# Optimization experiments

Hardware: AMD Instinct MI355X
Metric: run time of the kernel (lower is better)

## Reference

```python
import jax, jax.numpy as jnp
import numpy as np

N, NF, D, GH, E, B = 4096, 128, 64, 64, 32768, 32
NG, STEPS = 3, 3  # n_gcn, set2set processing steps


def setup_inputs() -> dict:
    key = jax.random.key(0)
    ks = iter(jax.random.split(key, 64))
    nrm = lambda shape: jax.random.normal(next(ks), shape, dtype=jnp.float32) * 0.05
    inp = {
        'x': jax.random.normal(next(ks), (N, NF), dtype=jnp.float32),
        'edge_attr': jax.random.uniform(next(ks), (E,), dtype=jnp.float32),
        'edge_idx': jax.random.randint(next(ks), (2, E), 0, N),
        'batch_map': jnp.sort(jax.random.randint(next(ks), (N,), 0, B)),
        # pre-GC MLP: NF->D, D->D, D->D (ReLU each)
        'pre_W0': nrm((NF, D)), 'pre_b0': nrm((D,)),
        'pre_W1': nrm((D, D)), 'pre_b1': nrm((D,)),
        'pre_W2': nrm((D, D)), 'pre_b2': nrm((D,)),
        # NNConv edge nets (stacked over NG layers): 1->GH->D*D
        'enn_W1': nrm((NG, 1, GH)), 'enn_b1': nrm((NG, GH)),
        'enn_W2': nrm((NG, GH, D * D)), 'enn_b2': nrm((NG, D * D)),
        'root_W': nrm((NG, D, D)), 'conv_b': nrm((NG, D)),
        # GRU(D, D) per layer, gate order r,z,n (torch), stored transposed for x@W
        'gru_Wih': nrm((NG, D, 3 * D)), 'gru_Whh': nrm((NG, D, 3 * D)),
        'gru_bih': nrm((NG, 3 * D)), 'gru_bhh': nrm((NG, 3 * D)),
        # Set2Set LSTM: input 2D -> hidden D, gate order i,f,g,o (torch)
        's2s_Wih': nrm((2 * D, 4 * D)), 's2s_Whh': nrm((D, 4 * D)),
        's2s_bih': nrm((4 * D,)), 's2s_bhh': nrm((4 * D,)),
        # post-GC MLP: 2D->D, D->D, D->D (ReLU each), then D->1
        'post_W0': nrm((2 * D, D)), 'post_b0': nrm((D,)),
        'post_W1': nrm((D, D)), 'post_b1': nrm((D,)),
        'post_W2': nrm((D, D)), 'post_b2': nrm((D,)),
        'post_W3': nrm((D, 1)), 'post_b3': nrm((1,)),
    }
    return inp


def _forward(x, edge_attr, pre_W0, pre_b0, pre_W1, pre_b1, pre_W2, pre_b2,
             enn_W1, enn_b1, enn_W2, enn_b2, root_W, conv_b,
             gru_Wih, gru_Whh, gru_bih, gru_bhh,
             s2s_Wih, s2s_Whh, s2s_bih, s2s_bhh,
             post_W0, post_b0, post_W1, post_b1, post_W2, post_b2,
             post_W3, post_b3, edge_idx, batch_map):
    relu, sig = jax.nn.relu, jax.nn.sigmoid
    # pre-GC layers
    out = relu(x @ pre_W0 + pre_b0)
    out = relu(out @ pre_W1 + pre_b1)
    out = relu(out @ pre_W2 + pre_b2)  # [N, D]

    src, dst = edge_idx[0], edge_idx[1]
    deg = jax.ops.segment_sum(jnp.ones((E,), out.dtype), dst, num_segments=N)
    deg = jnp.maximum(deg, 1.0)
    ea = edge_attr[:, None]  # view(-1, 1)

    for l in range(NG):
        h = out
        # NNConv: per-edge weight matrix from edge MLP
        We = relu(ea @ enn_W1[l] + enn_b1[l])              # [E, GH]
        We = (We @ enn_W2[l] + enn_b2[l]).reshape(E, D, D)  # [E, D, D]
        msg = jnp.einsum('ei,eio->eo', out[src], We)        # [E, D]
        agg = jax.ops.segment_sum(msg, dst, num_segments=N) / deg[:, None]
        conv = relu(agg + out @ root_W[l] + conv_b[l])
        # single-step GRU update (torch gate order r, z, n)
        gi = conv @ gru_Wih[l] + gru_bih[l]
        gh = h @ gru_Whh[l] + gru_bhh[l]
        i_r, i_z, i_n = jnp.split(gi, 3, axis=-1)
        h_r, h_z, h_n = jnp.split(gh, 3, axis=-1)
        r = sig(i_r + h_r)
        z = sig(i_z + h_z)
        n = jnp.tanh(i_n + r * h_n)
        out = (1.0 - z) * n + z * h

    # Set2Set pooling (early)
    q_star = jnp.zeros((B, 2 * D), out.dtype)
    hh = jnp.zeros((B, D), out.dtype)
    cc = jnp.zeros((B, D), out.dtype)
    for _ in range(STEPS):
        gates = q_star @ s2s_Wih + s2s_bih + hh @ s2s_Whh + s2s_bhh
        gi_, gf, gg, go = jnp.split(gates, 4, axis=-1)
        cc = sig(gf) * cc + sig(gi_) * jnp.tanh(gg)
        hh = sig(go) * jnp.tanh(cc)
        q = hh
        e = jnp.sum(out * q[batch_map], axis=-1)                    # [N]
        m = jax.ops.segment_max(e, batch_map, num_segments=B)
        a = jnp.exp(e - m[batch_map])
        den = jax.ops.segment_sum(a, batch_map, num_segments=B)
        a = a / den[batch_map]
        r_read = jax.ops.segment_sum(a[:, None] * out, batch_map, num_segments=B)
        q_star = jnp.concatenate([q, r_read], axis=-1)              # [B, 2D]

    # post-GC layers
    y = relu(q_star @ post_W0 + post_b0)
    y = relu(y @ post_W1 + post_b1)
    y = relu(y @ post_W2 + post_b2)
    y = y @ post_W3 + post_b3  # [B, 1]
    return y


def reference(x, edge_attr, edge_idx, batch_map, pre_W0, pre_b0, pre_W1, pre_b1,
              pre_W2, pre_b2, enn_W1, enn_b1, enn_W2, enn_b2, root_W, conv_b,
              gru_Wih, gru_Whh, gru_bih, gru_bhh, s2s_Wih, s2s_Whh, s2s_bih,
              s2s_bhh, post_W0, post_b0, post_W1, post_b1, post_W2, post_b2,
              post_W3, post_b3):
    return _forward(x, edge_attr, pre_W0, pre_b0, pre_W1, pre_b1, pre_W2, pre_b2,
                    enn_W1, enn_b1, enn_W2, enn_b2, root_W, conv_b,
                    gru_Wih, gru_Whh, gru_bih, gru_bhh,
                    s2s_Wih, s2s_Whh, s2s_bih, s2s_bhh,
                    post_W0, post_b0, post_W1, post_b1, post_W2, post_b2,
                    post_W3, post_b3, edge_idx, batch_map)
```

## Files before the change

kernel.cpp:

```cpp
#include <hip/hip_runtime.h>
#include <hip/hip_bf16.h>
#include <string.h>

#define NN   4096
#define NE   32768
#define NB   32
#define BKT  64

typedef __attribute__((ext_vector_type(8))) short short8;
typedef __attribute__((ext_vector_type(4))) float f4;

__device__ __forceinline__ float sigf(float x) { return 1.0f / (1.0f + __expf(-x)); }
__device__ __forceinline__ float bf2f(short s) {
    union { unsigned u; float f; } x;
    x.u = ((unsigned)(unsigned short)s) << 16;
    return x.f;
}
__device__ __forceinline__ short f2bf(float f) {
    __hip_bfloat16 h = __float2bfloat16(f);
    short s;
    memcpy(&s, &h, sizeof(short));
    return s;
}

__global__ __launch_bounds__(256) void k_setup(const float* __restrict__ x,
        const float* __restrict__ W0, const float* __restrict__ b0,
        const float* __restrict__ W1, const float* __restrict__ b1,
        const float* __restrict__ W2, const float* __restrict__ b2,
        const float* __restrict__ enn_W2, __hip_bfloat16* __restrict__ W2T,
        float* __restrict__ out, int* cnt_src, int* cnt_dst, int* bstart, int* bend) {
    int bid = blockIdx.x, t = threadIdx.x;
    if (bid < 32) {
        int i = bid * 256 + t;
        if (i < NN) cnt_src[i] = 0;
        else cnt_dst[i - NN] = 0;
        if (i < NB) { bstart[i] = 0x7FFFFFFF; bend[i] = 0; }
    } else if (bid < 224) {
        __shared__ __hip_bfloat16 tile[64 * 65];
        size_t base = (size_t)(bid - 32) * 4096;
        for (int i = t; i < 4096; i += 256) {
            int k = i >> 6, o = i & 63;
            tile[o * 65 + k] = __float2bfloat16(enn_W2[base + i]);
        }
        __syncthreads();
        for (int i = t; i < 4096; i += 256) {
            int o = i >> 6, k = i & 63;
            W2T[base + i] = tile[o * 65 + k];
        }
    } else {
        __shared__ float xr[4][128], ha[4][64], hb[4][64];
        int w = t >> 6, j = t & 63;
        int n = (bid - 224) * 4 + w;
        xr[w][j] = x[(size_t)n * 128 + j];
        xr[w][64 + j] = x[(size_t)n * 128 + 64 + j];
        float s = b0[j];
        #pragma unroll 8
        for (int k = 0; k < 128; ++k) s = fmaf(xr[w][k], W0[k * 64 + j], s);
        ha[w][j] = fmaxf(s, 0.f);
        s = b1[j];
        #pragma unroll 8
        for (int k = 0; k < 64; ++k) s = fmaf(ha[w][k], W1[k * 64 + j], s);
        hb[w][j] = fmaxf(s, 0.f);
        s = b2[j];
        #pragma unroll 8
        for (int k = 0; k < 64; ++k) s = fmaf(hb[w][k], W2[k * 64 + j], s);
        out[(size_t)n * 64 + j] = fmaxf(s, 0.f);
    }
}

__global__ __launch_bounds__(256, 4) void k_gemmPbt(const float* __restrict__ out,
        const __hip_bfloat16* __restrict__ W2T_l, const float* __restrict__ b2l,
        __hip_bfloat16* __restrict__ P, float* __restrict__ BT, float* __restrict__ agg,
        const int* __restrict__ eidx, const float* __restrict__ ea,
        const int* __restrict__ bm, int* cnt_src, int* cnt_dst,
        int* csr_dst, float* csr_ea, int* bstart, int* bend) {
    int bid = blockIdx.x, t = threadIdx.x;
    if (bid < 1024) {
        int mtile32 = bid >> 3, gchunk = bid & 7;
        int wave = t >> 6, lane = t & 63;
        int laneM = lane & 15, quad = lane >> 4;
        int rowhalf = wave & 1, subpair = wave >> 1;
        int arow = mtile32 * 32 + rowhalf * 16 + laneM;
        const float* Arow = out + (size_t)arow * 64;
        f4 af0 = *(const f4*)(Arow + quad * 8);
        f4 af1 = *(const f4*)(Arow + quad * 8 + 4);
        f4 af2 = *(const f4*)(Arow + 32 + quad * 8);
        f4 af3 = *(const f4*)(Arow + 32 + quad * 8 + 4);
        short8 a0, a1;
        #pragma unroll
        for (int j = 0; j < 4; ++j) {
            a0[j] = f2bf(af0[j]); a0[4 + j] = f2bf(af1[j]);
            a1[j] = f2bf(af2[j]); a1[4 + j] = f2bf(af3[j]);
        }
        #pragma unroll
        for (int sp = 0; sp < 2; ++sp) {
            int o0 = (subpair * 2 + sp) * 16;
            float accs[4][8];
            #pragma unroll
            for (int gg = 0; gg < 8; ++gg) {
                const __hip_bfloat16* Bt = W2T_l + (size_t)(gchunk * 8 + gg) * 4096;
                short8 b0v = *(const short8*)(Bt + (o0 + laneM) * 64 + quad * 8);
                short8 b1v = *(const short8*)(Bt + (o0 + laneM) * 64 + 32 + quad * 8);
                f4 acc = {0.f, 0.f, 0.f, 0.f};
                acc = __builtin_amdgcn_mfma_f32_16x16x32_bf16(a0, b0v, acc, 0, 0, 0);
                acc = __builtin_amdgcn_mfma_f32_16x16x32_bf16(a1, b1v, acc, 0, 0, 0);
                #pragma unroll
                for (int r = 0; r < 4; ++r) accs[r][gg] = acc[r];
            }
            int rowg = mtile32 * 32 + rowhalf * 16 + quad * 4;
            #pragma unroll
            for (int r = 0; r < 4; ++r) {
                short8 sv;
                #pragma unroll
                for (int j = 0; j < 8; ++j)
                    sv[j] = f2bf(accs[r][j]);
                *(short8*)(P + (size_t)(rowg + r) * 4096 + gchunk * 512
                             + (o0 + laneM) * 8) = sv;
            }
        }
    } else if (bid < 2048) {
        __shared__ float sh[4][64];
        int w = t >> 6, j = t & 63;
        int n = (bid - 1024) * 4 + w;
        sh[w][j] = out[(size_t)n * 64 + j];
        agg[(size_t)n * 64 + j] = 0.f;
        __syncthreads();
        float s = 0.f;
        #pragma unroll 8
        for (int k = 0; k < 64; ++k) s = fmaf(sh[w][k], b2l[k * 64 + j], s);
        BT[(size_t)n * 64 + j] = s;
    } else {
        int e = (bid - 2048) * 256 + t;
        if (e < NE) {
            int s = eidx[e];
            int d = eidx[NE + e];
            int slot = atomicAdd(&cnt_src[s], 1);
            if (slot < BKT) {
                csr_dst[s * BKT + slot] = d;
                csr_ea[s * BKT + slot] = ea[e];
            }
            atomicAdd(&cnt_dst[d], 1);
        }
        if (e < NN) {
            int b = bm[e];
            atomicMin(&bstart[b], e);
            atomicMax(&bend[b], e + 1);
        }
    }
}

#define MSG_CHUNK 32
__global__ __launch_bounds__(256, 2) void k_msg(const __hip_bfloat16* __restrict__ P,
        const float* __restrict__ BT, const int* __restrict__ cnt_src,
        const int* __restrict__ csr_dst, const float* __restrict__ csr_ea,
        const float* __restrict__ W1l, const float* __restrict__ b1l,
        float* __restrict__ agg) {
    __shared__ float wlds[4][MSG_CHUNK][64];
    int t = threadIdx.x, wave = t >> 6, lane = t & 63;
    int n = blockIdx.x * 4 + wave;
    int deg = cnt_src[n];
    if (deg > BKT) deg = BKT;
    float w1v = W1l[lane], b1v = b1l[lane];
    float preg[64];
    const __hip_bfloat16* Pn = P + (size_t)n * 4096 + lane * 8;
    #pragma unroll
    for (int c = 0; c < 8; ++c) {
        short8 v = *(const short8*)(Pn + c * 512);
        #pragma unroll
        for (int j = 0; j < 8; ++j) preg[c * 8 + j] = bf2f(v[j]);
    }
    float bt = BT[(size_t)n * 64 + lane];
    const int* bdst = csr_dst + n * BKT;
    const float* bea = csr_ea + n * BKT;
    for (int c0 = 0; c0 < deg; c0 += MSG_CHUNK) {
        int cc = deg - c0; if (cc > MSG_CHUNK) cc = MSG_CHUNK;
        for (int si = 0; si < cc; ++si) {
            float eav = bea[c0 + si];
            wlds[wave][si][lane] = fmaxf(fmaf(eav, w1v, b1v), 0.f);
        }
        for (int i = 0; i < cc; ++i) {
            int dst = bdst[c0 + i];
            const float* wr = wlds[wave][i];
            float acc0 = bt, acc1 = 0.f, acc2 = 0.f, acc3 = 0.f;
            #pragma unroll
            for (int g = 0; g < 64; g += 16) {
                float4 w0 = *(const float4*)(wr + g);
                float4 w1 = *(const float4*)(wr + g + 4);
                float4 w2 = *(const float4*)(wr + g + 8);
                float4 w3 = *(const float4*)(wr + g + 12);
                acc0 = fmaf(w0.x, preg[g], acc0);
                acc0 = fmaf(w0.y, preg[g + 1], acc0);
                acc0 = fmaf(w0.z, preg[g + 2], acc0);
                acc0 = fmaf(w0.w, preg[g + 3], acc0);
                acc1 = fmaf(w1.x, preg[g + 4], acc1);
                acc1 = fmaf(w1.y, preg[g + 5], acc1);
                acc1 = fmaf(w1.z, preg[g + 6], acc1);
                acc1 = fmaf(w1.w, preg[g + 7], acc1);
                acc2 = fmaf(w2.x, preg[g + 8], acc2);
                acc2 = fmaf(w2.y, preg[g + 9], acc2);
                acc2 = fmaf(w2.z, preg[g + 10], acc2);
                acc2 = fmaf(w2.w, preg[g + 11], acc2);
                acc3 = fmaf(w3.x, preg[g + 12], acc3);
                acc3 = fmaf(w3.y, preg[g + 13], acc3);
                acc3 = fmaf(w3.z, preg[g + 14], acc3);
                acc3 = fmaf(w3.w, preg[g + 15], acc3);
            }
            float acc = (acc0 + acc1) + (acc2 + acc3);
            atomicAdd(&agg[(size_t)dst * 64 + lane], acc);
        }
    }
}

__global__ __launch_bounds__(256) void k_gru(const float* __restrict__ out,
        const float* __restrict__ agg, const int* __restrict__ cnt_dst,
        const float* __restrict__ rootW, const float* __restrict__ convb,
        const float* __restrict__ Wih, const float* __restrict__ Whh,
        const float* __restrict__ bih, const float* __restrict__ bhh,
        float* __restrict__ outn) {
    __shared__ float sh[4][64], sc[4][64];
    int t = threadIdx.x, w = t >> 6, j = t & 63;
    int n = blockIdx.x * 4 + w;
    float hj = out[(size_t)n * 64 + j];
    sh[w][j] = hj;
    int dg = cnt_dst[n];
    float invd = 1.0f / (float)(dg > 0 ? dg : 1);
    __syncthreads();
    float s = agg[(size_t)n * 64 + j] * invd + convb[j];
    #pragma unroll 8
    for (int k = 0; k < 64; ++k) s = fmaf(sh[w][k], rootW[k * 64 + j], s);
    float conv = fmaxf(s, 0.f);
    sc[w][j] = conv;
    __syncthreads();
    float gir = bih[j], giz = bih[64 + j], gin = bih[128 + j];
    float ghr = bhh[j], ghz = bhh[64 + j], ghn = bhh[128 + j];
    #pragma unroll 4
    for (int k = 0; k < 64; ++k) {
        float c = sc[w][k], h = sh[w][k];
        gir = fmaf(c, Wih[k * 192 + j], gir);
        giz = fmaf(c, Wih[k * 192 + 64 + j], giz);
        gin = fmaf(c, Wih[k * 192 + 128 + j], gin);
        ghr = fmaf(h, Whh[k * 192 + j], ghr);
        ghz = fmaf(h, Whh[k * 192 + 64 + j], ghz);
        ghn = fmaf(h, Whh[k * 192 + 128 + j], ghn);
    }
    float r = sigf(gir + ghr);
    float z = sigf(giz + ghz);
    float nn = tanhf(gin + r * ghn);
    outn[(size_t)n * 64 + j] = (1.f - z) * nn + z * hj;
}

__global__ __launch_bounds__(1024) void k_s2s_post(const float* __restrict__ out,
        const int* __restrict__ bstart, const int* __restrict__ bend,
        const float* __restrict__ Wih, const float* __restrict__ Whh,
        const float* __restrict__ bih, const float* __restrict__ bhh,
        const float* __restrict__ pW0, const float* __restrict__ pb0,
        const float* __restrict__ pW1, const float* __restrict__ pb1,
        const float* __restrict__ pW2, const float* __restrict__ pb2,
        const float* __restrict__ pW3, const float* __restrict__ pb3,
        float* __restrict__ y) {
    __shared__ float cache[192 * 65];
    __shared__ float qs[128], hh[64], cc[64], gates[256];
    __shared__ float ebuf[1024];
    __shared__ float redbuf[1024];
    __shared__ float redw[16];
    __shared__ float smax, sinv;
    __shared__ float tmp64[64];
    int t = threadIdx.x, wave = t >> 6, lane = t & 63;
    int b = blockIdx.x;
    int s0 = bstart[b], e0 = bend[b];
    int cnt = e0 - s0;
    if (cnt < 0) cnt = 0;
    if (cnt > 1024) cnt = 1024;
    int ccnt = cnt < 192 ? cnt : 192;
    for (int li = t; li < ccnt * 64; li += 1024) {
        int rowi = li >> 6, d = li & 63;
        cache[rowi * 65 + d] = out[(size_t)(s0 + rowi) * 64 + d];
    }
    int g = t & 255, seg = t >> 8;
    const float* wp;
    int kcnt;
    if (seg == 0)      { wp = Wih + g;             kcnt = 64; }
    else if (seg == 1) { wp = Wih + 64 * 256 + g;  kcnt = 64; }
    else if (seg == 2) { wp = Whh + g;             kcnt = 32; }
    else               { wp = Whh + 32 * 256 + g;  kcnt = 32; }
    float wreg[64];
    #pragma unroll
    for (int j = 0; j < 64; ++j)
        wreg[j] = (j < kcnt) ? wp[(size_t)j * 256] : 0.f;
    if (t < 128) qs[t] = 0.f;
    if (t < 64) { hh[t] = 0.f; cc[t] = 0.f; }
    __syncthreads();
    for (int step = 0; step < 3; ++step) {
        const float* vsrc = (seg == 0) ? qs : (seg == 1) ? qs + 64
                          : (seg == 2) ? hh : hh + 32;
        float partial = 0.f;
        #pragma unroll
        for (int j = 0; j < 64; ++j)
            if (j < kcnt) partial = fmaf(vsrc[j], wreg[j], partial);
        redbuf[seg * 256 + g] = partial;
        __syncthreads();
        if (t < 256)
            gates[t] = bih[t] + bhh[t] + redbuf[t] + redbuf[256 + t]
                     + redbuf[512 + t] + redbuf[768 + t];
        __syncthreads();
        if (t < 64) {
            float cn = sigf(gates[64 + t]) * cc[t] + sigf(gates[t]) * tanhf(gates[128 + t]);
            cc[t] = cn;
            hh[t] = sigf(gates[192 + t]) * tanhf(cn);
        }
        __syncthreads();
        for (int idx = t; idx < cnt; idx += 1024) {
            float s = 0.f;
            if (idx < 192) {
                const float* row = cache + idx * 65;
                #pragma unroll 8
                for (int d = 0; d < 64; ++d) s = fmaf(row[d], hh[d], s);
            } else {
                const float* row = out + (size_t)(s0 + idx) * 64;
                for (int d = 0; d < 64; ++d) s = fmaf(row[d], hh[d], s);
            }
            ebuf[idx] = s;
        }
        __syncthreads();
        float lm = (t < cnt) ? ebuf[t] : -3.0e38f;
        #pragma unroll
        for (int off = 32; off > 0; off >>= 1) lm = fmaxf(lm, __shfl_down(lm, off, 64));
        if (lane == 0) redw[wave] = lm;
        __syncthreads();
        if (t == 0) {
            float m = redw[0];
            #pragma unroll
            for (int w2 = 1; w2 < 16; ++w2) m = fmaxf(m, redw[w2]);
            smax = m;
        }
        __syncthreads();
        float m = smax;
        float av = 0.f;
        if (t < cnt) {
            av = __expf(ebuf[t] - m);
            ebuf[t] = av;
        }
        float ls = av;
        #pragma unroll
        for (int off = 32; off > 0; off >>= 1) ls += __shfl_down(ls, off, 64);
        if (lane == 0) redw[wave] = ls;
        __syncthreads();
        if (t == 0) {
            float s = 0.f;
            #pragma unroll
            for (int w2 = 0; w2 < 16; ++w2) s += redw[w2];
            sinv = (cnt > 0) ? 1.f / s : 0.f;
        }
        __syncthreads();
        float inv = sinv;
        float r = 0.f;
        for (int idx = wave; idx < cnt; idx += 16) {
            float a = ebuf[idx];
            float v = (idx < 192) ? cache[idx * 65 + lane]
                                  : out[(size_t)(s0 + idx) * 64 + lane];
            r = fmaf(a, v, r);
        }
        redbuf[wave * 64 + lane] = r;
        __syncthreads();
        if (t < 64) {
            float s = 0.f;
            #pragma unroll
            for (int w2 = 0; w2 < 16; ++w2) s += redbuf[w2 * 64 + t];
            qs[64 + t] = s * inv;
            qs[t] = hh[t];
        }
        __syncthreads();
    }
    if (t < 64) {
        float s = pb0[t];
        #pragma unroll 4
        for (int k = 0; k < 128; ++k) s = fmaf(qs[k], pW0[k * 64 + t], s);
        tmp64[t] = fmaxf(s, 0.f);
    }
    __syncthreads();
    float h1v = 0.f;
    if (t < 64) {
        float s = pb1[t];
        #pragma unroll 4
        for (int k = 0; k < 64; ++k) s = fmaf(tmp64[k], pW1[k * 64 + t], s);
        h1v = fmaxf(s, 0.f);
    }
    __syncthreads();
    if (t < 64) tmp64[t] = h1v;
    __syncthreads();
    if (t < 64) {
        float s = pb2[t];
        #pragma unroll 4
        for (int k = 0; k < 64; ++k) s = fmaf(tmp64[k], pW2[k * 64 + t], s);
        gates[t] = fmaxf(s, 0.f) * pW3[t];
    }
    __syncthreads();
    if (t == 0) {
        float yy = pb3[0];
        for (int k = 0; k < 64; ++k) yy += gates[k];
        y[b] = yy;
    }
}


extern "C" void kernel_launch(void* const* d_in, const int* in_sizes, int n_in,
                              void* d_out, int out_size, void* d_ws, size_t ws_size,
                              hipStream_t stream) {
    const float* x         = (const float*)d_in[0];
    const float* edge_attr = (const float*)d_in[1];
    const int*   edge_idx  = (const int*)d_in[2];
    const int*   batch_map = (const int*)d_in[3];
    const float* pre_W0 = (const float*)d_in[4];
    const float* pre_b0 = (const float*)d_in[5];
    const float* pre_W1 = (const float*)d_in[6];
    const float* pre_b1 = (const float*)d_in[7];
    const float* pre_W2 = (const float*)d_in[8];
    const float* pre_b2 = (const float*)d_in[9];
    const float* enn_W1 = (const float*)d_in[10];
    const float* enn_b1 = (const float*)d_in[11];
    const float* enn_W2 = (const float*)d_in[12];
    const float* enn_b2 = (const float*)d_in[13];
    const float* root_W = (const float*)d_in[14];
    const float* conv_b = (const float*)d_in[15];
    const float* gru_Wih = (const float*)d_in[16];
    const float* gru_Whh = (const float*)d_in[17];
    const float* gru_bih = (const float*)d_in[18];
    const float* gru_bhh = (const float*)d_in[19];
    const float* s2s_Wih = (const float*)d_in[20];
    const float* s2s_Whh = (const float*)d_in[21];
    const float* s2s_bih = (const float*)d_in[22];
    const float* s2s_bhh = (const float*)d_in[23];
    const float* post_W0 = (const float*)d_in[24];
    const float* post_b0 = (const float*)d_in[25];
    const float* post_W1 = (const float*)d_in[26];
    const float* post_b1 = (const float*)d_in[27];
    const float* post_W2 = (const float*)d_in[28];
    const float* post_b2 = (const float*)d_in[29];
    const float* post_W3 = (const float*)d_in[30];
    const float* post_b3 = (const float*)d_in[31];
    float* yout = (float*)d_out;

    char* wp = (char*)d_ws;
    auto take = [&](size_t bytes) -> char* {
        char* r = wp;
        wp += (bytes + 255) & ~(size_t)255;
        return r;
    };
    float* outA = (float*)take((size_t)NN * 64 * 4);
    float* outB = (float*)take((size_t)NN * 64 * 4);
    __hip_bfloat16* P = (__hip_bfloat16*)take((size_t)NN * 4096 * 2);
    float* BT  = (float*)take((size_t)NN * 64 * 4);
    float* agg = (float*)take((size_t)NN * 64 * 4);
    __hip_bfloat16* W2T = (__hip_bfloat16*)take((size_t)3 * 64 * 4096 * 2);
    int* cnt_src  = (int*)take((size_t)NN * 4);
    int* cnt_dst  = (int*)take((size_t)NN * 4);
    int* csr_dst  = (int*)take((size_t)NN * BKT * 4);
    float* csr_ea = (float*)take((size_t)NN * BKT * 4);
    int* bstart   = (int*)take((size_t)NB * 4);
    int* bend     = (int*)take((size_t)NB * 4);

    k_setup<<<1248, 256, 0, stream>>>(x, pre_W0, pre_b0, pre_W1, pre_b1, pre_W2, pre_b2,
                                      enn_W2, W2T, outA, cnt_src, cnt_dst, bstart, bend);

    float* cur = outA;
    float* nxt = outB;
    for (int l = 0; l < 3; ++l) {
        int grid = (l == 0) ? 2176 : 2048;
        k_gemmPbt<<<grid, 256, 0, stream>>>(cur, W2T + (size_t)l * 64 * 4096,
                                            enn_b2 + (size_t)l * 4096, P, BT, agg,
                                            edge_idx, edge_attr, batch_map,
                                            cnt_src, cnt_dst, csr_dst, csr_ea,
                                            bstart, bend);
        k_msg<<<NN / 4, 256, 0, stream>>>(P, BT, cnt_src, csr_dst, csr_ea,
                                          enn_W1 + l * 64, enn_b1 + l * 64, agg);
        k_gru<<<NN / 4, 256, 0, stream>>>(cur, agg, cnt_dst, root_W + l * 4096,
                                          conv_b + l * 64, gru_Wih + l * 64 * 192,
                                          gru_Whh + l * 64 * 192, gru_bih + l * 192,
                                          gru_bhh + l * 192, nxt);
        float* tmp = cur; cur = nxt; nxt = tmp;
    }
    k_s2s_post<<<NB, 1024, 0, stream>>>(cur, bstart, bend, s2s_Wih, s2s_Whh, s2s_bih,
                                        s2s_bhh, post_W0, post_b0, post_W1, post_b1,
                                        post_W2, post_b2, post_W3, post_b3, yout);
}
```

Baseline: 373.5 us.

## Fuse edge-weight GEMM into message passing, keep per-node P in LDS

```diff
diff --git a/kernel.cpp b/kernel.cpp
--- a/kernel.cpp
+++ b/kernel.cpp
@@ -6,29 +6,30 @@
 #define NE   32768
 #define NB   32
 #define BKT  64
+#define FN   8
 
 typedef __attribute__((ext_vector_type(8))) short short8;
 typedef __attribute__((ext_vector_type(4))) float f4;
 
 __device__ __forceinline__ float sigf(float x) { return 1.0f / (1.0f + __expf(-x)); }
-__device__ __forceinline__ float bf2f(short s) {
-    union { unsigned u; float f; } x;
-    x.u = ((unsigned)(unsigned short)s) << 16;
-    return x.f;
-}
 __device__ __forceinline__ short f2bf(float f) {
     __hip_bfloat16 h = __float2bfloat16(f);
     short s;
     memcpy(&s, &h, sizeof(short));
     return s;
 }
+__device__ __forceinline__ unsigned packbf2(float lo, float hi) {
+    return (unsigned)(unsigned short)f2bf(lo) | ((unsigned)(unsigned short)f2bf(hi) << 16);
+}
 
 __global__ __launch_bounds__(256) void k_setup(const float* __restrict__ x,
         const float* __restrict__ W0, const float* __restrict__ b0,
         const float* __restrict__ W1, const float* __restrict__ b1,
         const float* __restrict__ W2, const float* __restrict__ b2,
-        const float* __restrict__ enn_W2, __hip_bfloat16* __restrict__ W2T,
-        float* __restrict__ out, int* cnt_src, int* cnt_dst, int* bstart, int* bend) {
+        const float* __restrict__ enn_W2, const float* __restrict__ b2e0,
+        __hip_bfloat16* __restrict__ W2T, float* __restrict__ out,
+        float* __restrict__ BT, float* __restrict__ agg,
+        int* cnt_src, int* cnt_dst, int* bstart, int* bend) {
     int bid = blockIdx.x, t = threadIdx.x;
     if (bid < 32) {
         int i = bid * 256 + t;
@@ -64,148 +65,114 @@
         s = b2[j];
         #pragma unroll 8
         for (int k = 0; k < 64; ++k) s = fmaf(hb[w][k], W2[k * 64 + j], s);
-        out[(size_t)n * 64 + j] = fmaxf(s, 0.f);
-    }
-}
-
-__global__ __launch_bounds__(256, 4) void k_gemmPbt(const float* __restrict__ out,
-        const __hip_bfloat16* __restrict__ W2T_l, const float* __restrict__ b2l,
-        __hip_bfloat16* __restrict__ P, float* __restrict__ BT, float* __restrict__ agg,
-        const int* __restrict__ eidx, const float* __restrict__ ea,
-        const int* __restrict__ bm, int* cnt_src, int* cnt_dst,
-        int* csr_dst, float* csr_ea, int* bstart, int* bend) {
-    int bid = blockIdx.x, t = threadIdx.x;
-    if (bid < 1024) {
-        int mtile32 = bid >> 3, gchunk = bid & 7;
-        int wave = t >> 6, lane = t & 63;
-        int laneM = lane & 15, quad = lane >> 4;
-        int rowhalf = wave & 1, subpair = wave >> 1;
-        int arow = mtile32 * 32 + rowhalf * 16 + laneM;
-        const float* Arow = out + (size_t)arow * 64;
-        f4 af0 = *(const f4*)(Arow + quad * 8);
-        f4 af1 = *(const f4*)(Arow + quad * 8 + 4);
-        f4 af2 = *(const f4*)(Arow + 32 + quad * 8);
-        f4 af3 = *(const f4*)(Arow + 32 + quad * 8 + 4);
-        short8 a0, a1;
+        float val = fmaxf(s, 0.f);
+        out[(size_t)n * 64 + j] = val;
+        ha[w][j] = val;
+        agg[(size_t)n * 64 + j] = 0.f;
+        float s2 = 0.f;
+        #pragma unroll 8
+        for (int k = 0; k < 64; ++k) s2 = fmaf(ha[w][k], b2e0[k * 64 + j], s2);
+        BT[(size_t)n * 64 + j] = s2;
+    }
+}
+
+__global__ __launch_bounds__(256) void k_edges(const int* __restrict__ eidx,
+        const float* __restrict__ ea, const int* __restrict__ bm,
+        int* cnt_src, int* cnt_dst, int* csr_dst, float* csr_ea,
+        int* bstart, int* bend) {
+    int e = blockIdx.x * 256 + threadIdx.x;
+    if (e < NE) {
+        int s = eidx[e];
+        int d = eidx[NE + e];
+        int slot = atomicAdd(&cnt_src[s], 1);
+        if (slot < BKT) {
+            csr_dst[s * BKT + slot] = d;
+            csr_ea[s * BKT + slot] = ea[e];
+        }
+        atomicAdd(&cnt_dst[d], 1);
+    }
+    if (e < NN) {
+        int b = bm[e];
+        atomicMin(&bstart[b], e);
+        atomicMax(&bend[b], e + 1);
+    }
+}
+
+__global__ __launch_bounds__(256, 2) void k_fused(const float* __restrict__ out,
+        const __hip_bfloat16* __restrict__ W2T_l, const float* __restrict__ BT,
+        const int* __restrict__ cnt_src, const int* __restrict__ csr_dst,
+        const float* __restrict__ csr_ea, const float* __restrict__ W1l,
+        const float* __restrict__ b1l, float* __restrict__ agg) {
+    __shared__ unsigned Plds[FN * 32 * 64];
+    int t = threadIdx.x, wave = t >> 6, lane = t & 63;
+    int laneM = lane & 15, quad = lane >> 4;
+    int n0 = blockIdx.x * FN;
+    const float* Arow = out + (size_t)(n0 + laneM) * 64;
+    f4 af0 = *(const f4*)(Arow + quad * 8);
+    f4 af1 = *(const f4*)(Arow + quad * 8 + 4);
+    f4 af2 = *(const f4*)(Arow + 32 + quad * 8);
+    f4 af3 = *(const f4*)(Arow + 32 + quad * 8 + 4);
+    short8 a0, a1;
+    #pragma unroll
+    for (int j = 0; j < 4; ++j) {
+        a0[j] = f2bf(af0[j]); a0[4 + j] = f2bf(af1[j]);
+        a1[j] = f2bf(af2[j]); a1[4 + j] = f2bf(af3[j]);
+    }
+    #pragma unroll
+    for (int gp = 0; gp < 8; ++gp) {
+        int g0 = wave * 16 + gp * 2;
+        const __hip_bfloat16* Bt0 = W2T_l + (size_t)g0 * 4096;
+        const __hip_bfloat16* Bt1 = Bt0 + 4096;
         #pragma unroll
-        for (int j = 0; j < 4; ++j) {
-            a0[j] = f2bf(af0[j]); a0[4 + j] = f2bf(af1[j]);
-            a1[j] = f2bf(af2[j]); a1[4 + j] = f2bf(af3[j]);
-        }
-        #pragma unroll
-        for (int sp = 0; sp < 2; ++sp) {
-            int o0 = (subpair * 2 + sp) * 16;
-            float accs[4][8];
+        for (int ot = 0; ot < 4; ++ot) {
+            int o0 = ot * 16;
+            short8 b00 = *(const short8*)(Bt0 + (o0 + laneM) * 64 + quad * 8);
+            short8 b01 = *(const short8*)(Bt0 + (o0 + laneM) * 64 + 32 + quad * 8);
+            short8 b10 = *(const short8*)(Bt1 + (o0 + laneM) * 64 + quad * 8);
+            short8 b11 = *(const short8*)(Bt1 + (o0 + laneM) * 64 + 32 + quad * 8);
+            f4 c0 = {0.f, 0.f, 0.f, 0.f};
+            f4 c1 = {0.f, 0.f, 0.f, 0.f};
+            c0 = __builtin_amdgcn_mfma_f32_16x16x32_bf16(a0, b00, c0, 0, 0, 0);
+            c0 = __builtin_amdgcn_mfma_f32_16x16x32_bf16(a1, b01, c0, 0, 0, 0);
+            c1 = __builtin_amdgcn_mfma_f32_16x16x32_bf16(a0, b10, c1, 0, 0, 0);
+            c1 = __builtin_amdgcn_mfma_f32_16x16x32_bf16(a1, b11, c1, 0, 0, 0);
+            if (quad < 2) {
+                #pragma unroll
+                for (int r = 0; r < 4; ++r) {
+                    int node = quad * 4 + r;
+                    Plds[(node * 32 + (g0 >> 1)) * 64 + o0 + laneM] = packbf2(c0[r], c1[r]);
+                }
+            }
+        }
+    }
+    __syncthreads();
+    float wcoef = W1l[lane], bcoef = b1l[lane];
+    #pragma unroll
+    for (int ni = 0; ni < 2; ++ni) {
+        int nloc = wave * 2 + ni;
+        int n = n0 + nloc;
+        int deg = cnt_src[n];
+        if (deg > BKT) deg = BKT;
+        float bt = BT[(size_t)n * 64 + lane];
+        const int* bdst = csr_dst + n * BKT;
+        const float* bea = csr_ea + n * BKT;
+        const unsigned* Pn = Plds + nloc * 2048;
+        for (int i = 0; i < deg; ++i) {
+            float eav = bea[i];
+            int dst = bdst[i];
+            float we = fmaxf(fmaf(eav, wcoef, bcoef), 0.f);
+            float acc = bt;
             #pragma unroll
-            for (int gg = 0; gg < 8; ++gg) {
-                const __hip_bfloat16* Bt = W2T_l + (size_t)(gchunk * 8 + gg) * 4096;
-                short8 b0v = *(const short8*)(Bt + (o0 + laneM) * 64 + quad * 8);
-                short8 b1v = *(const short8*)(Bt + (o0 + laneM) * 64 + 32 + quad * 8);
-                f4 acc = {0.f, 0.f, 0.f, 0.f};
-                acc = __builtin_amdgcn_mfma_f32_16x16x32_bf16(a0, b0v, acc, 0, 0, 0);
-                acc = __builtin_amdgcn_mfma_f32_16x16x32_bf16(a1, b1v, acc, 0, 0, 0);
-                #pragma unroll
-                for (int r = 0; r < 4; ++r) accs[r][gg] = acc[r];
+            for (int g2 = 0; g2 < 32; ++g2) {
+                unsigned pv = Pn[g2 * 64 + lane];
+                union { unsigned u; float f; } lo, hi;
+                lo.u = pv << 16;
+                hi.u = pv & 0xFFFF0000u;
+                float w0 = __shfl(we, g2 * 2, 64);
+                float w1 = __shfl(we, g2 * 2 + 1, 64);
+                acc = fmaf(w0, lo.f, acc);
+                acc = fmaf(w1, hi.f, acc);
             }
-            int rowg = mtile32 * 32 + rowhalf * 16 + quad * 4;
-            #pragma unroll
-            for (int r = 0; r < 4; ++r) {
-                short8 sv;
-                #pragma unroll
-                for (int j = 0; j < 8; ++j)
-                    sv[j] = f2bf(accs[r][j]);
-                *(short8*)(P + (size_t)(rowg + r) * 4096 + gchunk * 512
-                             + (o0 + laneM) * 8) = sv;
-            }
-        }
-    } else if (bid < 2048) {
-        __shared__ float sh[4][64];
-        int w = t >> 6, j = t & 63;
-        int n = (bid - 1024) * 4 + w;
-        sh[w][j] = out[(size_t)n * 64 + j];
-        agg[(size_t)n * 64 + j] = 0.f;
-        __syncthreads();
-        float s = 0.f;
-        #pragma unroll 8
-        for (int k = 0; k < 64; ++k) s = fmaf(sh[w][k], b2l[k * 64 + j], s);
-        BT[(size_t)n * 64 + j] = s;
-    } else {
-        int e = (bid - 2048) * 256 + t;
-        if (e < NE) {
-            int s = eidx[e];
-            int d = eidx[NE + e];
-            int slot = atomicAdd(&cnt_src[s], 1);
-            if (slot < BKT) {
-                csr_dst[s * BKT + slot] = d;
-                csr_ea[s * BKT + slot] = ea[e];
-            }
-            atomicAdd(&cnt_dst[d], 1);
-        }
-        if (e < NN) {
-            int b = bm[e];
-            atomicMin(&bstart[b], e);
-            atomicMax(&bend[b], e + 1);
-        }
-    }
-}
-
-#define MSG_CHUNK 32
-__global__ __launch_bounds__(256, 2) void k_msg(const __hip_bfloat16* __restrict__ P,
-        const float* __restrict__ BT, const int* __restrict__ cnt_src,
-        const int* __restrict__ csr_dst, const float* __restrict__ csr_ea,
-        const float* __restrict__ W1l, const float* __restrict__ b1l,
-        float* __restrict__ agg) {
-    __shared__ float wlds[4][MSG_CHUNK][64];
-    int t = threadIdx.x, wave = t >> 6, lane = t & 63;
-    int n = blockIdx.x * 4 + wave;
-    int deg = cnt_src[n];
-    if (deg > BKT) deg = BKT;
-    float w1v = W1l[lane], b1v = b1l[lane];
-    float preg[64];
-    const __hip_bfloat16* Pn = P + (size_t)n * 4096 + lane * 8;
-    #pragma unroll
-    for (int c = 0; c < 8; ++c) {
-        short8 v = *(const short8*)(Pn + c * 512);
-        #pragma unroll
-        for (int j = 0; j < 8; ++j) preg[c * 8 + j] = bf2f(v[j]);
-    }
-    float bt = BT[(size_t)n * 64 + lane];
-    const int* bdst = csr_dst + n * BKT;
-    const float* bea = csr_ea + n * BKT;
-    for (int c0 = 0; c0 < deg; c0 += MSG_CHUNK) {
-        int cc = deg - c0; if (cc > MSG_CHUNK) cc = MSG_CHUNK;
-        for (int si = 0; si < cc; ++si) {
-            float eav = bea[c0 + si];
-            wlds[wave][si][lane] = fmaxf(fmaf(eav, w1v, b1v), 0.f);
-        }
-        for (int i = 0; i < cc; ++i) {
-            int dst = bdst[c0 + i];
-            const float* wr = wlds[wave][i];
-            float acc0 = bt, acc1 = 0.f, acc2 = 0.f, acc3 = 0.f;
-            #pragma unroll
-            for (int g = 0; g < 64; g += 16) {
-                float4 w0 = *(const float4*)(wr + g);
-                float4 w1 = *(const float4*)(wr + g + 4);
-                float4 w2 = *(const float4*)(wr + g + 8);
-                float4 w3 = *(const float4*)(wr + g + 12);
-                acc0 = fmaf(w0.x, preg[g], acc0);
-                acc0 = fmaf(w0.y, preg[g + 1], acc0);
-                acc0 = fmaf(w0.z, preg[g + 2], acc0);
-                acc0 = fmaf(w0.w, preg[g + 3], acc0);
-                acc1 = fmaf(w1.x, preg[g + 4], acc1);
-                acc1 = fmaf(w1.y, preg[g + 5], acc1);
-                acc1 = fmaf(w1.z, preg[g + 6], acc1);
-                acc1 = fmaf(w1.w, preg[g + 7], acc1);
-                acc2 = fmaf(w2.x, preg[g + 8], acc2);
-                acc2 = fmaf(w2.y, preg[g + 9], acc2);
-                acc2 = fmaf(w2.z, preg[g + 10], acc2);
-                acc2 = fmaf(w2.w, preg[g + 11], acc2);
-                acc3 = fmaf(w3.x, preg[g + 12], acc3);
-                acc3 = fmaf(w3.y, preg[g + 13], acc3);
-                acc3 = fmaf(w3.z, preg[g + 14], acc3);
-                acc3 = fmaf(w3.w, preg[g + 15], acc3);
-            }
-            float acc = (acc0 + acc1) + (acc2 + acc3);
             atomicAdd(&agg[(size_t)dst * 64 + lane], acc);
         }
     }
@@ -216,7 +183,8 @@
         const float* __restrict__ rootW, const float* __restrict__ convb,
         const float* __restrict__ Wih, const float* __restrict__ Whh,
         const float* __restrict__ bih, const float* __restrict__ bhh,
-        float* __restrict__ outn) {
+        const float* __restrict__ b2next, float* __restrict__ BT,
+        float* __restrict__ aggz, float* __restrict__ outn) {
     __shared__ float sh[4][64], sc[4][64];
     int t = threadIdx.x, w = t >> 6, j = t & 63;
     int n = blockIdx.x * 4 + w;
@@ -245,8 +213,17 @@
     }
     float r = sigf(gir + ghr);
     float z = sigf(giz + ghz);
-    float nn = tanhf(gin + r * ghn);
-    outn[(size_t)n * 64 + j] = (1.f - z) * nn + z * hj;
+    float nnv = tanhf(gin + r * ghn);
+    float val = (1.f - z) * nnv + z * hj;
+    outn[(size_t)n * 64 + j] = val;
+    if (b2next) {
+        sh[w][j] = val;
+        aggz[(size_t)n * 64 + j] = 0.f;
+        float s2 = 0.f;
+        #pragma unroll 8
+        for (int k = 0; k < 64; ++k) s2 = fmaf(sh[w][k], b2next[k * 64 + j], s2);
+        BT[(size_t)n * 64 + j] = s2;
+    }
 }
 
 __global__ __launch_bounds__(1024) void k_s2s_post(const float* __restrict__ out,
@@ -448,7 +425,6 @@
     };
     float* outA = (float*)take((size_t)NN * 64 * 4);
     float* outB = (float*)take((size_t)NN * 64 * 4);
-    __hip_bfloat16* P = (__hip_bfloat16*)take((size_t)NN * 4096 * 2);
     float* BT  = (float*)take((size_t)NN * 64 * 4);
     float* agg = (float*)take((size_t)NN * 64 * 4);
     __hip_bfloat16* W2T = (__hip_bfloat16*)take((size_t)3 * 64 * 4096 * 2);
@@ -460,23 +436,23 @@
     int* bend     = (int*)take((size_t)NB * 4);
 
     k_setup<<<1248, 256, 0, stream>>>(x, pre_W0, pre_b0, pre_W1, pre_b1, pre_W2, pre_b2,
-                                      enn_W2, W2T, outA, cnt_src, cnt_dst, bstart, bend);
+                                      enn_W2, enn_b2, W2T, outA, BT, agg,
+                                      cnt_src, cnt_dst, bstart, bend);
+    k_edges<<<NE / 256, 256, 0, stream>>>(edge_idx, edge_attr, batch_map,
+                                          cnt_src, cnt_dst, csr_dst, csr_ea,
+                                          bstart, bend);
 
     float* cur = outA;
     float* nxt = outB;
     for (int l = 0; l < 3; ++l) {
-        int grid = (l == 0) ? 2176 : 2048;
-        k_gemmPbt<<<grid, 256, 0, stream>>>(cur, W2T + (size_t)l * 64 * 4096,
-                                            enn_b2 + (size_t)l * 4096, P, BT, agg,
-                                            edge_idx, edge_attr, batch_map,
-                                            cnt_src, cnt_dst, csr_dst, csr_ea,
-                                            bstart, bend);
-        k_msg<<<NN / 4, 256, 0, stream>>>(P, BT, cnt_src, csr_dst, csr_ea,
-                                          enn_W1 + l * 64, enn_b1 + l * 64, agg);
+        k_fused<<<NN / FN, 256, 0, stream>>>(cur, W2T + (size_t)l * 64 * 4096, BT,
+                                             cnt_src, csr_dst, csr_ea,
+                                             enn_W1 + l * 64, enn_b1 + l * 64, agg);
+        const float* b2next = (l < 2) ? (enn_b2 + (size_t)(l + 1) * 4096) : nullptr;
         k_gru<<<NN / 4, 256, 0, stream>>>(cur, agg, cnt_dst, root_W + l * 4096,
                                           conv_b + l * 64, gru_Wih + l * 64 * 192,
                                           gru_Whh + l * 64 * 192, gru_bih + l * 192,
-                                          gru_bhh + l * 192, nxt);
+                                          gru_bhh + l * 192, b2next, BT, agg, nxt);
         float* tmp = cur; cur = nxt; nxt = tmp;
     }
     k_s2s_post<<<NB, 1024, 0, stream>>>(cur, bstart, bend, s2s_Wih, s2s_Whh, s2s_bih,
```

New measurement: 458.3 us. 22.7% more time.
